# Kernel tuning notes

Hardware: AMD Instinct MI355X
Metric: run time of the kernel (lower is better)

## Reference

```python
import jax, jax.numpy as jnp
import numpy as np

B, S, D, H = 4, 2048, 1024, 16
HD = D // H
FF = 4 * D
EPS = 1e-5


def _layer_norm(x, w, b):
    mu = jnp.mean(x, axis=-1, keepdims=True)
    var = jnp.mean(jnp.square(x - mu), axis=-1, keepdims=True)
    return (x - mu) * jax.lax.rsqrt(var + EPS) * w + b


def setup_inputs() -> dict:
    key = jax.random.key(0)
    ks = jax.random.split(key, 8)
    std = 0.02
    return {
        "x": jax.random.normal(ks[0], (B, S, D), dtype=jnp.float32),
        "ln1_w": jnp.ones((D,), jnp.float32),
        "ln1_b": jnp.zeros((D,), jnp.float32),
        "w_qkv": jax.random.normal(ks[1], (D, 3 * D), dtype=jnp.float32) * std,  # fused QKV, no bias
        "w_proj": jax.random.normal(ks[2], (D, D), dtype=jnp.float32) * std,
        "b_proj": jnp.zeros((D,), jnp.float32),
        "ln2_w": jnp.ones((D,), jnp.float32),
        "ln2_b": jnp.zeros((D,), jnp.float32),
        "w_ff1": jax.random.normal(ks[3], (D, FF), dtype=jnp.float32) * std,
        "b_ff1": jnp.zeros((FF,), jnp.float32),
        "w_ff2": jax.random.normal(ks[4], (FF, D), dtype=jnp.float32) * std,
        "b_ff2": jnp.zeros((D,), jnp.float32),
    }


def reference(x, ln1_w, ln1_b, w_qkv, w_proj, b_proj, ln2_w, ln2_b, w_ff1, b_ff1, w_ff2, b_ff2):
    b, s, d = x.shape
    # --- attention branch (pre-LN) ---
    h = _layer_norm(x, ln1_w, ln1_b)
    kqv = (h @ w_qkv).reshape(b, s, H, HD, 3)  # fused projection, split by last index
    k, q, v = kqv[..., 0], kqv[..., 1], kqv[..., 2]  # each [b, s, H, HD]
    scores = jnp.einsum("bqhd,bkhd->bhqk", q, k) * (HD ** -0.5)  # [b,H,s,s]
    causal = jnp.tril(jnp.ones((s, s), dtype=bool))
    scores = jnp.where(causal, scores, -jnp.inf)
    weights = jax.nn.softmax(scores, axis=-1)
    ctx = jnp.einsum("bhqk,bkhd->bqhd", weights, v).reshape(b, s, d)
    attn_out = ctx @ w_proj + b_proj
    x = x + attn_out
    # --- feed-forward branch (pre-LN) ---
    h = _layer_norm(x, ln2_w, ln2_b)
    ff = jax.nn.gelu(h @ w_ff1 + b_ff1, approximate=False) @ w_ff2 + b_ff2
    return x + ff
```

## Files before the change

kernel.cpp:

```cpp
#include <hip/hip_runtime.h>

typedef unsigned short u16;
typedef unsigned int u32;
typedef __bf16 bf16x8 __attribute__((ext_vector_type(8)));
typedef float f32x4 __attribute__((ext_vector_type(4)));
typedef float f32x16 __attribute__((ext_vector_type(16)));
typedef unsigned short us8 __attribute__((ext_vector_type(8)));
typedef unsigned short us4 __attribute__((ext_vector_type(4)));
typedef unsigned int u32x4 __attribute__((ext_vector_type(4)));

#define B_ 4
#define S_ 2048
#define D_ 1024
#define H_ 16
#define HD_ 64
#define QKS_ 3072
#define EPS_ 1e-5f
#define SCALE_ (0.125f * 1.44269504088896341f)
#define THR_ 3.0f

__device__ __forceinline__ u16 f2bf(float f) {
  unsigned u = __builtin_bit_cast(unsigned, f);
  u = (u + 0x7FFFu + ((u >> 16) & 1u)) >> 16;
  return (u16)u;
}

__device__ __forceinline__ float gelu_f(float x) {
  float u = x * (2.3022388f + 0.10294971f * x * x);
  float te = __builtin_amdgcn_exp2f(u);
  return x - x * __builtin_amdgcn_rcpf(1.0f + te);
}

typedef const __attribute__((address_space(1))) unsigned int* gp1;
typedef __attribute__((address_space(3))) unsigned int* lp3;
__device__ __forceinline__ void gl_lds16(const void* g, void* l) {
  __builtin_amdgcn_global_load_lds((gp1)(unsigned long long)g,
                                   (lp3)(unsigned int)(unsigned long long)l,
                                   16, 0, 0);
}

__device__ __forceinline__ u32 cvtpk_bf16(float lo, float hi) {
  u32 d;
  asm("v_cvt_pk_bf16_f32 %0, %1, %2" : "=v"(d) : "v"(lo), "v"(hi));
  return d;
}
__device__ __forceinline__ void swap32(u32& a, u32& b) {
  asm("v_permlane32_swap_b32 %0, %1" : "+v"(a), "+v"(b));
}

__device__ __forceinline__ f32x16 zero16() {
  f32x16 z;
#pragma unroll
  for (int i = 0; i < 16; i++) z[i] = 0.f;
  return z;
}

__global__ __launch_bounds__(256) void wconv_kernel(const float* __restrict__ W,
                                                    u16* __restrict__ Wt,
                                                    int Kd, int N, int perm) {
  __shared__ u16 tile[32][33];
  int bid = blockIdx.x;
  int nbn = N >> 5;
  int tk = bid / nbn, tn = bid % nbn;
  int tx = threadIdx.x & 31, ty = threadIdx.x >> 5;
#pragma unroll
  for (int i = 0; i < 4; i++) {
    int r = ty + i * 8;
    tile[r][tx] = f2bf(W[(size_t)(tk * 32 + r) * N + tn * 32 + tx]);
  }
  __syncthreads();
#pragma unroll
  for (int i = 0; i < 4; i++) {
    int r = ty + i * 8;
    int orow = tn * 32 + r;
    int prow = perm ? ((orow % 3) << 10) + orow / 3 : orow;
    Wt[(size_t)prow * Kd + tk * 32 + tx] = tile[tx][r];
  }
}

__global__ __launch_bounds__(256) void vtrans_kernel(const u16* __restrict__ kqv,
                                                     u16* __restrict__ Vt) {
  __shared__ u16 tile[64][72];
  int bh = blockIdx.x >> 5;
  int sb = blockIdx.x & 31;
  int b = bh >> 4, h = bh & 15;
  const u16* src = kqv + ((size_t)(b * S_ + sb * 64)) * QKS_ + 2048 + h * 64;
  int r = threadIdx.x >> 2, c0 = (threadIdx.x & 3) * 16;
  *(us8*)&tile[r][c0] = *(const us8*)(src + (size_t)r * QKS_ + c0);
  *(us8*)&tile[r][c0 + 8] = *(const us8*)(src + (size_t)r * QKS_ + c0 + 8);
  __syncthreads();
  u16* dst = Vt + (size_t)bh * HD_ * S_ + sb * 64;
  int hd = threadIdx.x >> 2;
  int s0 = (threadIdx.x & 3) * 16;
  us8 a, bb;
#pragma unroll
  for (int j = 0; j < 8; j++) a[j] = tile[s0 + j][hd];
#pragma unroll
  for (int j = 0; j < 8; j++) bb[j] = tile[s0 + 8 + j][hd];
  *(us8*)(dst + (size_t)hd * S_ + s0) = a;
  *(us8*)(dst + (size_t)hd * S_ + s0 + 8) = bb;
}

__global__ __launch_bounds__(256) void ln_kernel(const float* __restrict__ x,
                                                 const float* __restrict__ w,
                                                 const float* __restrict__ b,
                                                 u16* __restrict__ out) {
  int row = blockIdx.x;
  int t = threadIdx.x;
  int lane = t & 63, wid = t >> 6;
  const float4* xr = (const float4*)(x + (size_t)row * D_);
  float4 v = xr[t];
  float s = v.x + v.y + v.z + v.w;
  float q = v.x * v.x + v.y * v.y + v.z * v.z + v.w * v.w;
#pragma unroll
  for (int off = 1; off < 64; off <<= 1) {
    s += __shfl_xor(s, off);
    q += __shfl_xor(q, off);
  }
  __shared__ float red[8];
  if (lane == 0) { red[wid] = s; red[4 + wid] = q; }
  __syncthreads();
  s = red[0] + red[1] + red[2] + red[3];
  q = red[4] + red[5] + red[6] + red[7];
  float mu = s * (1.0f / D_);
  float var = q * (1.0f / D_) - mu * mu;
  float rs = rsqrtf(var + EPS_);
  int c = t * 4;
  float4 wv = *(const float4*)(w + c);
  float4 bv = *(const float4*)(b + c);
  us4 o;
  o[0] = f2bf((v.x - mu) * rs * wv.x + bv.x);
  o[1] = f2bf((v.y - mu) * rs * wv.y + bv.y);
  o[2] = f2bf((v.z - mu) * rs * wv.z + bv.z);
  o[3] = f2bf((v.w - mu) * rs * wv.w + bv.w);
  *(us4*)(out + (size_t)row * D_ + c) = o;
}

template <int MODE>
__global__ __launch_bounds__(256) void gemm_kernel(
    const u16* __restrict__ A, const u16* __restrict__ Bt,
    const float* __restrict__ bias, const float* __restrict__ res,
    float* __restrict__ Cf, u16* __restrict__ Cb,
    int M, int N, int K) {
  __shared__ __align__(16) u16 Al[128 * 64];
  __shared__ __align__(16) u16 Bl[128 * 64];
  int t = threadIdx.x;
  int nbn = N >> 7;
  int nwg = gridDim.x, cpx = nwg >> 3;
  int bid = (blockIdx.x & 7) * cpx + (blockIdx.x >> 3);
  int nsn = nbn >> 3;
  int st = bid >> 6, u = bid & 63;
  int bm = (st / nsn) * 8 + (u >> 3);
  int bn = (st % nsn) * 8 + (u & 7);
  int lane = t & 63, wid = t >> 6;
  int wm = wid >> 1, wn = wid & 1;
  int lrow = lane & 15, lgr = lane >> 4;
  int sl7 = lrow & 7;
  const u16* Ab = A + (size_t)bm * 128 * K;
  const u16* Bb = Bt + (size_t)bn * 128 * K;
  int sr = lane >> 3;
  int sc = ((lane & 7) ^ sr) << 3;
  const u16* Ag[4];
  const u16* Bg[4];
  u16* Ald[4];
  u16* Bld[4];
#pragma unroll
  for (int j = 0; j < 4; j++) {
    int row0 = (j * 4 + wid) * 8;
    Ag[j] = Ab + (size_t)(row0 + sr) * K + sc;
    Bg[j] = Bb + (size_t)(row0 + sr) * K + sc;
    Ald[j] = &Al[row0 * 64 + lane * 8];
    Bld[j] = &Bl[row0 * 64 + lane * 8];
  }
  f32x4 acc[4][4] = {};
  for (int k0 = 0; k0 < K; k0 += 64) {
#pragma unroll
    for (int j = 0; j < 4; j++) {
      gl_lds16(Ag[j] + k0, Ald[j]);
      gl_lds16(Bg[j] + k0, Bld[j]);
    }
    __syncthreads();
    bf16x8 af[2][4], bfr[2][4];
#pragma unroll
    for (int ks = 0; ks < 2; ks++) {
      int slot = ((ks << 2) | lgr) ^ sl7;
#pragma unroll
      for (int m = 0; m < 4; m++)
        af[ks][m] = *(const bf16x8*)&Al[(wm * 64 + m * 16 + lrow) * 64 + slot * 8];
#pragma unroll
      for (int n = 0; n < 4; n++)
        bfr[ks][n] = *(const bf16x8*)&Bl[(wn * 64 + n * 16 + lrow) * 64 + slot * 8];
    }
    __builtin_amdgcn_s_setprio(1);
#pragma unroll
    for (int m = 0; m < 4; m++)
#pragma unroll
      for (int n = 0; n < 4; n++) {
        acc[m][n] = __builtin_amdgcn_mfma_f32_16x16x32_bf16(af[0][m], bfr[0][n], acc[m][n], 0, 0, 0);
        acc[m][n] = __builtin_amdgcn_mfma_f32_16x16x32_bf16(af[1][m], bfr[1][n], acc[m][n], 0, 0, 0);
      }
    __builtin_amdgcn_s_setprio(0);
    __syncthreads();
  }
#pragma unroll
  for (int n = 0; n < 4; n++) {
    int col = bn * 128 + wn * 64 + n * 16 + lrow;
    float bv = (MODE & 1) ? bias[col] : 0.0f;
#pragma unroll
    for (int m = 0; m < 4; m++)
#pragma unroll
      for (int r = 0; r < 4; r++) {
        int row = bm * 128 + wm * 64 + m * 16 + lgr * 4 + r;
        float v = acc[m][n][r] + bv;
        if (MODE & 2) v = gelu_f(v);
        if (MODE & 4) v += res[(size_t)row * N + col];
        if (MODE & 8) Cb[(size_t)row * N + col] = f2bf(v);
        else          Cf[(size_t)row * N + col] = v;
      }
  }
}

__device__ __forceinline__ void attn_softmax_update(
    f32x16* s, int NSUB_rt, float& mrun, float& lrun, f32x16 (&o)[2], int hi) {
  float pmax = -3.0e38f;
  for (int sub = 0; sub < NSUB_rt; sub++)
#pragma unroll
    for (int r = 0; r < 16; r++) pmax = fmaxf(pmax, s[sub][r]);
  pmax = fmaxf(pmax, __shfl_xor(pmax, 32));
  bool ok = (pmax * SCALE_ <= mrun + THR_);
  if (!__all(ok)) {
    float mnew = fmaxf(mrun, pmax * SCALE_);
    float corr = __builtin_amdgcn_exp2f(mrun - mnew);
    mrun = mnew;
    lrun *= corr;
#pragma unroll
    for (int r = 0; r < 16; r++) {
      float cr = __shfl(corr, ((r & 3) + 8 * (r >> 2)) + 4 * hi);
      o[0][r] *= cr;
      o[1][r] *= cr;
    }
  }
  float m = mrun;
  float lacc = 0.f;
  for (int sub = 0; sub < NSUB_rt; sub++)
#pragma unroll
    for (int r = 0; r < 16; r++) {
      float p = __builtin_amdgcn_exp2f(__builtin_fmaf(s[sub][r], SCALE_, -m));
      s[sub][r] = p;
      lacc += p;
    }
  lrun += lacc;
}

__device__ __forceinline__ void attn_pfrag(const f32x16& s, bf16x8& pa, bf16x8& pb) {
  u32 a0 = cvtpk_bf16(s[0], s[1]);
  u32 a1 = cvtpk_bf16(s[2], s[3]);
  u32 a2 = cvtpk_bf16(s[4], s[5]);
  u32 a3 = cvtpk_bf16(s[6], s[7]);
  swap32(a0, a2);
  swap32(a1, a3);
  u32 b0 = cvtpk_bf16(s[8], s[9]);
  u32 b1 = cvtpk_bf16(s[10], s[11]);
  u32 b2 = cvtpk_bf16(s[12], s[13]);
  u32 b3 = cvtpk_bf16(s[14], s[15]);
  swap32(b0, b2);
  swap32(b1, b3);
  u32x4 fa = {a0, a1, a2, a3};
  u32x4 fb = {b0, b1, b2, b3};
  pa = __builtin_bit_cast(bf16x8, fa);
  pb = __builtin_bit_cast(bf16x8, fb);
}

template <bool MASK>
__device__ __forceinline__ void attn_chunk_tail(
    const u16* __restrict__ Kh, const u16* __restrict__ Vh,
    const bf16x8 (&qf)[4], f32x16 (&o)[2],
    float& mrun, float& lrun, int kb, int qrow, int hi, int ln31) {
  f32x16 s[1];
  f32x16 z = zero16();
  __builtin_amdgcn_s_setprio(1);
#pragma unroll
  for (int ks = 0; ks < 4; ks++) {
    bf16x8 kfr = *(const bf16x8*)(Kh + (size_t)(kb + ln31) * QKS_ + ks * 16 + hi * 8);
    z = __builtin_amdgcn_mfma_f32_32x32x16_bf16(kfr, qf[ks], z, 0, 0, 0);
  }
  __builtin_amdgcn_s_setprio(0);
  if (MASK) {
#pragma unroll
    for (int r = 0; r < 16; r++) {
      int key = kb + (r & 3) + 8 * (r >> 2) + 4 * hi;
      if (key > qrow) z[r] = -3.0e38f;
    }
  }
  s[0] = z;
  attn_softmax_update(s, 1, mrun, lrun, o, hi);
  bf16x8 pa, pb;
  attn_pfrag(s[0], pa, pb);
  __builtin_amdgcn_s_setprio(1);
#pragma unroll
  for (int ht = 0; ht < 2; ht++) {
    const u16* vb = Vh + (size_t)(ht * 32 + ln31) * S_ + kb + hi * 8;
    bf16x8 v1 = *(const bf16x8*)(vb);
    bf16x8 v2 = *(const bf16x8*)(vb + 16);
    o[ht] = __builtin_amdgcn_mfma_f32_32x32x16_bf16(pa, v1, o[ht], 0, 0, 0);
    o[ht] = __builtin_amdgcn_mfma_f32_32x32x16_bf16(pb, v2, o[ht], 0, 0, 0);
  }
  __builtin_amdgcn_s_setprio(0);
}

__global__ __launch_bounds__(256) void attn_kernel(const u16* __restrict__ kqv,
                                                   const u16* __restrict__ Vt,
                                                   u16* __restrict__ ctx) {
  __shared__ __align__(16) u16 Kl[2][64 * 64];
  __shared__ __align__(16) u16 Vl[2][64 * 64];
  int t = threadIdx.x;
  int lane = t & 63, wid = t >> 6;
  int qblk = 15 - (int)(blockIdx.x >> 6);
  int bh = blockIdx.x & 63;
  int b = bh >> 4, h = bh & 15;
  const u16* Qh = kqv + (size_t)b * S_ * QKS_ + 1024 + h * 64;
  const u16* Kh = kqv + (size_t)b * S_ * QKS_ + h * 64;
  const u16* Vh = Vt + (size_t)bh * HD_ * S_;
  int qb = qblk * 128;
  int qbase = qb + wid * 32;
  int ln31 = lane & 31, hi = lane >> 5;
  int qrow = qbase + ln31;
  int l7 = ln31 & 7;

  int srow = t >> 3;
  int sslot = (t & 7) ^ (srow & 7);
  const u16* Ksrc = Kh + (size_t)srow * QKS_ + sslot * 8;
  const u16* Vsrc = Vh + (size_t)srow * S_ + sslot * 8;

  auto stageK = [&](int kb1, int buf) {
    gl_lds16(Ksrc + (size_t)kb1 * QKS_, &Kl[buf][t * 8]);
    gl_lds16(Ksrc + (size_t)(kb1 + 32) * QKS_, &Kl[buf][2048 + t * 8]);
  };
  auto stageV = [&](int kb1, int buf) {
    gl_lds16(Vsrc + kb1, &Vl[buf][t * 8]);
    gl_lds16(Vsrc + (size_t)32 * S_ + kb1, &Vl[buf][2048 + t * 8]);
  };

  bf16x8 qf[4];
#pragma unroll
  for (int ks = 0; ks < 4; ks++)
    qf[ks] = *(const bf16x8*)(Qh + (size_t)qrow * QKS_ + ks * 16 + hi * 8);

  f32x16 o[2] = {zero16(), zero16()};
  float mrun = -1.0e30f, lrun = 0.f;

  int nf64 = qbase >> 6;
  int NT = (qb >> 6) + 2;

  stageK(0, 0);
  stageV(0, 0);
  for (int kt = 0; kt < NT; kt++) {
    int cur = kt & 1;
    if (kt + 1 < NT) {
      int kb1 = (kt + 1) * 64;
      stageK(kb1, cur ^ 1);
      stageV(kb1, cur ^ 1);
      asm volatile("s_waitcnt vmcnt(4)" ::: "memory");
    } else {
      asm volatile("s_waitcnt vmcnt(0)" ::: "memory");
    }
    __builtin_amdgcn_sched_barrier(0);
    __builtin_amdgcn_s_barrier();
    __builtin_amdgcn_sched_barrier(0);
    if (kt < nf64) {
      const u16* Kc = &Kl[cur][0];
      const u16* Vc = &Vl[cur][0];
      f32x16 s[2];
#pragma unroll
      for (int sub = 0; sub < 2; sub++) {
        f32x16 z = zero16();
        __builtin_amdgcn_s_setprio(1);
#pragma unroll
        for (int ks = 0; ks < 4; ks++) {
          int kr = sub * 32 + ln31;
          int sl = (ks * 2 + hi) ^ l7;
          bf16x8 kfr = *(const bf16x8*)&Kc[kr * 64 + sl * 8];
          z = __builtin_amdgcn_mfma_f32_32x32x16_bf16(kfr, qf[ks], z, 0, 0, 0);
        }
        __builtin_amdgcn_s_setprio(0);
        s[sub] = z;
      }
      attn_softmax_update(s, 2, mrun, lrun, o, hi);
#pragma unroll
      for (int sub = 0; sub < 2; sub++) {
        bf16x8 pa, pb;
        attn_pfrag(s[sub], pa, pb);
        __builtin_amdgcn_s_setprio(1);
#pragma unroll
        for (int ht = 0; ht < 2; ht++) {
          int vr = ht * 32 + ln31;
          int s1 = (sub * 4 + hi) ^ (vr & 7);
          int s2 = (sub * 4 + hi + 2) ^ (vr & 7);
          bf16x8 v1 = *(const bf16x8*)&Vc[vr * 64 + s1 * 8];
          bf16x8 v2 = *(const bf16x8*)&Vc[vr * 64 + s2 * 8];
          o[ht] = __builtin_amdgcn_mfma_f32_32x32x16_bf16(pa, v1, o[ht], 0, 0, 0);
          o[ht] = __builtin_amdgcn_mfma_f32_32x32x16_bf16(pb, v2, o[ht], 0, 0, 0);
        }
        __builtin_amdgcn_s_setprio(0);
      }
    }
    __builtin_amdgcn_sched_barrier(0);
    __builtin_amdgcn_s_barrier();
    __builtin_amdgcn_sched_barrier(0);
  }

  if (qbase & 32)
    attn_chunk_tail<false>(Kh, Vh, qf, o, mrun, lrun, qbase - 32, qrow, hi, ln31);
  attn_chunk_tail<true>(Kh, Vh, qf, o, mrun, lrun, qbase, qrow, hi, ln31);

  float l = lrun + __shfl_xor(lrun, 32);
  float inv = 1.0f / l;
#pragma unroll
  for (int r = 0; r < 16; r++) {
    float invr = __shfl(inv, ((r & 3) + 8 * (r >> 2)) + 4 * hi);
    int q = qbase + (r & 3) + 8 * (r >> 2) + 4 * hi;
    size_t base = ((size_t)b * S_ + q) * D_ + h * HD_;
    ctx[base + ln31] = f2bf(o[0][r] * invr);
    ctx[base + 32 + ln31] = f2bf(o[1][r] * invr);
  }
}

extern "C" void kernel_launch(void* const* d_in, const int* in_sizes, int n_in,
                              void* d_out, int out_size, void* d_ws, size_t ws_size,
                              hipStream_t stream) {
  const float* x = (const float*)d_in[0];
  const float* ln1w = (const float*)d_in[1];
  const float* ln1b = (const float*)d_in[2];
  const float* wqkv = (const float*)d_in[3];
  const float* wproj = (const float*)d_in[4];
  const float* bproj = (const float*)d_in[5];
  const float* ln2w = (const float*)d_in[6];
  const float* ln2b = (const float*)d_in[7];
  const float* wff1 = (const float*)d_in[8];
  const float* bff1 = (const float*)d_in[9];
  const float* wff2 = (const float*)d_in[10];
  const float* bff2 = (const float*)d_in[11];

  char* ws = (char*)d_ws;
  u16* wqkvT = (u16*)(ws + 0);
  u16* wprojT = (u16*)(ws + 6291456);
  u16* wff1T = (u16*)(ws + 8388608);
  u16* wff2T = (u16*)(ws + 16777216);
  u16* h1 = (u16*)(ws + 25165824);
  u16* Vt = (u16*)(ws + 25165824);
  u16* kqv = (u16*)(ws + 41943040);
  u16* ctx = (u16*)(ws + 92274688);
  float* x1 = (float*)(ws + 109051904);
  u16* h2 = (u16*)(ws + 142606336);
  u16* g = (u16*)(ws + 25165824);
  float* outp = (float*)d_out;

  wconv_kernel<<<(1024 / 32) * (3072 / 32), 256, 0, stream>>>(wqkv, wqkvT, 1024, 3072, 1);
  wconv_kernel<<<(1024 / 32) * (1024 / 32), 256, 0, stream>>>(wproj, wprojT, 1024, 1024, 0);
  wconv_kernel<<<(1024 / 32) * (4096 / 32), 256, 0, stream>>>(wff1, wff1T, 1024, 4096, 0);
  wconv_kernel<<<(4096 / 32) * (1024 / 32), 256, 0, stream>>>(wff2, wff2T, 4096, 1024, 0);

  ln_kernel<<<8192, 256, 0, stream>>>(x, ln1w, ln1b, h1);
  gemm_kernel<8><<<1536, 256, 0, stream>>>(h1, wqkvT, nullptr, nullptr, nullptr, kqv,
                                           8192, 3072, 1024);
  vtrans_kernel<<<64 * 32, 256, 0, stream>>>(kqv, Vt);
  attn_kernel<<<16 * 64, 256, 0, stream>>>(kqv, Vt, ctx);
  gemm_kernel<5><<<512, 256, 0, stream>>>(ctx, wprojT, bproj, x, x1, nullptr,
                                          8192, 1024, 1024);
  ln_kernel<<<8192, 256, 0, stream>>>(x1, ln2w, ln2b, h2);
  gemm_kernel<11><<<2048, 256, 0, stream>>>(h2, wff1T, bff1, nullptr, nullptr, g,
                                            8192, 4096, 1024);
  gemm_kernel<5><<<512, 256, 0, stream>>>(g, wff2T, bff2, x1, outp, nullptr,
                                          8192, 1024, 4096);
}
```

Measured before the change: 346.2 us.

## Add 8-wave ping-pong GEMM with larger tiles for FFN matmuls

```diff
diff --git a/kernel.cpp b/kernel.cpp
--- a/kernel.cpp
+++ b/kernel.cpp
@@ -220,6 +220,151 @@
   }
 }
 
+#define VWAIT(n) asm volatile("s_waitcnt vmcnt(" #n ")" ::: "memory")
+
+#define LDA(AF, MQ)                                                             \
+  _Pragma("unroll") for (int ks = 0; ks < 2; ks++) {                            \
+    int slot = ((((ks << 2) | lgr) ^ sl7)) * 8;                                 \
+    _Pragma("unroll") for (int m = 0; m < MH; m++)                              \
+      AF[ks][m] = *(const bf16x8*)&Ac[((MQ) * (BM / 2) + wm * (BM / 4) +        \
+                                       m * 16 + lrow) * 64 + slot];             \
+  }
+
+#define LDB(BF, NQ)                                                             \
+  _Pragma("unroll") for (int ks = 0; ks < 2; ks++) {                            \
+    int slot = ((((ks << 2) | lgr) ^ sl7)) * 8;                                 \
+    _Pragma("unroll") for (int nn = 0; nn < 2; nn++)                            \
+      BF[ks][nn] = *(const bf16x8*)&Bc[((NQ) * 128 + wn * 32 + nn * 16 +        \
+                                        lrow) * 64 + slot];                     \
+  }
+
+#define BARR_MFMA(MQ, NQ, AF, BF)                                               \
+  __builtin_amdgcn_s_barrier();                                                 \
+  asm volatile("s_waitcnt lgkmcnt(0)" ::: "memory");                            \
+  __builtin_amdgcn_sched_barrier(0);                                            \
+  __builtin_amdgcn_s_setprio(1);                                                \
+  _Pragma("unroll") for (int m = 0; m < MH; m++)                                \
+    _Pragma("unroll") for (int nn = 0; nn < 2; nn++) {                          \
+      acc[MQ][NQ][m][nn] = __builtin_amdgcn_mfma_f32_16x16x32_bf16(             \
+          AF[0][m], BF[0][nn], acc[MQ][NQ][m][nn], 0, 0, 0);                    \
+      acc[MQ][NQ][m][nn] = __builtin_amdgcn_mfma_f32_16x16x32_bf16(             \
+          AF[1][m], BF[1][nn], acc[MQ][NQ][m][nn], 0, 0, 0);                    \
+    }                                                                           \
+  __builtin_amdgcn_s_setprio(0);                                                \
+  __builtin_amdgcn_s_barrier();
+
+template <int MODE, int BM>
+__global__ __launch_bounds__(512) void gemm8p_kernel(
+    const u16* __restrict__ A, const u16* __restrict__ Bt,
+    const float* __restrict__ bias, const float* __restrict__ res,
+    float* __restrict__ Cf, u16* __restrict__ Cb,
+    int M, int N, int K) {
+  constexpr int LA = BM / 128;
+  constexpr int MH = BM / 64;
+  constexpr int ASZ = BM * 64;
+  constexpr int BSZ = 256 * 64;
+  extern __shared__ __align__(16) u16 sm[];
+  int t = threadIdx.x;
+  int nbn = N >> 8;
+  int nwg = gridDim.x, cpx = nwg >> 3;
+  int bid = (blockIdx.x % 8) * cpx + blockIdx.x / 8;
+  int bm = bid / nbn, bn = bid % nbn;
+  int lane = t & 63, wid = t >> 6;
+  int wm = wid >> 2, wn = wid & 3;
+  int lrow = lane & 15, lgr = lane >> 4;
+  int sl7 = lrow & 7;
+  const u16* Ab = A + (size_t)bm * BM * K;
+  const u16* Bb = Bt + (size_t)bn * 256 * K;
+  int srt = t >> 3;
+  int ssc = (((t & 7) ^ (srt & 7)) << 3);
+  const u16* Asrc = Ab + (size_t)srt * K + ssc;
+  const u16* Bsrc = Bb + (size_t)srt * K + ssc;
+
+  auto stageA = [&](int kt, int bsel, int h) {
+    int k0 = kt * 64;
+    u16* dst = sm + bsel * (ASZ + BSZ) + (h * (BM / 2)) * 64 + t * 8;
+#pragma unroll
+    for (int a = 0; a < LA; a++)
+      gl_lds16(Asrc + (size_t)(h * (BM / 2) + a * 64) * K + k0, dst + a * 4096);
+  };
+  auto stageB = [&](int kt, int bsel, int h) {
+    int k0 = kt * 64;
+    u16* dst = sm + bsel * (ASZ + BSZ) + ASZ + (h * 128) * 64 + t * 8;
+#pragma unroll
+    for (int b2 = 0; b2 < 2; b2++)
+      gl_lds16(Bsrc + (size_t)(h * 128 + b2 * 64) * K + k0, dst + b2 * 4096);
+  };
+
+  f32x4 acc[2][2][MH][2] = {};
+  int NT = K >> 6;
+  stageA(0, 0, 0);
+  stageB(0, 0, 0);
+  stageB(0, 0, 1);
+  stageA(0, 0, 1);
+  if constexpr (BM == 256) VWAIT(4); else VWAIT(3);
+  __builtin_amdgcn_s_barrier();
+  for (int kt = 0; kt < NT - 1; kt++) {
+    int cur = kt & 1, nb = cur ^ 1;
+    const u16* Ac = sm + cur * (ASZ + BSZ);
+    const u16* Bc = Ac + ASZ;
+    bf16x8 af[2][MH], bf[2][2];
+    LDA(af, 0);
+    LDB(bf, 0);
+    stageA(kt + 1, nb, 0);
+    if constexpr (BM == 256) VWAIT(4); else VWAIT(2);
+    BARR_MFMA(0, 0, af, bf);
+    LDB(bf, 1);
+    stageB(kt + 1, nb, 0);
+    if constexpr (BM == 256) VWAIT(4); else VWAIT(3);
+    BARR_MFMA(0, 1, af, bf);
+    LDA(af, 1);
+    stageB(kt + 1, nb, 1);
+    BARR_MFMA(1, 1, af, bf);
+    LDB(bf, 0);
+    stageA(kt + 1, nb, 1);
+    if constexpr (BM == 256) VWAIT(4); else VWAIT(3);
+    BARR_MFMA(1, 0, af, bf);
+  }
+  {
+    int cur = (NT - 1) & 1;
+    const u16* Ac = sm + cur * (ASZ + BSZ);
+    const u16* Bc = Ac + ASZ;
+    bf16x8 af[2][MH], bf[2][2];
+    LDA(af, 0);
+    LDB(bf, 0);
+    if constexpr (BM == 256) VWAIT(2); else VWAIT(1);
+    BARR_MFMA(0, 0, af, bf);
+    LDB(bf, 1);
+    VWAIT(0);
+    BARR_MFMA(0, 1, af, bf);
+    LDA(af, 1);
+    BARR_MFMA(1, 1, af, bf);
+    LDB(bf, 0);
+    BARR_MFMA(1, 0, af, bf);
+  }
+#pragma unroll
+  for (int nq = 0; nq < 2; nq++) {
+#pragma unroll
+    for (int nn = 0; nn < 2; nn++) {
+      int col = bn * 256 + nq * 128 + wn * 32 + nn * 16 + lrow;
+      float bv = (MODE & 1) ? bias[col] : 0.0f;
+#pragma unroll
+      for (int mq = 0; mq < 2; mq++)
+#pragma unroll
+        for (int m = 0; m < MH; m++)
+#pragma unroll
+          for (int r = 0; r < 4; r++) {
+            int row = bm * BM + mq * (BM / 2) + wm * (BM / 4) + m * 16 + lgr * 4 + r;
+            float v = acc[mq][nq][m][nn][r] + bv;
+            if (MODE & 2) v = gelu_f(v);
+            if (MODE & 4) v += res[(size_t)row * N + col];
+            if (MODE & 8) Cb[(size_t)row * N + col] = f2bf(v);
+            else          Cf[(size_t)row * N + col] = v;
+          }
+    }
+  }
+}
+
 __device__ __forceinline__ void attn_softmax_update(
     f32x16* s, int NSUB_rt, float& mrun, float& lrun, f32x16 (&o)[2], int hi) {
   float pmax = -3.0e38f;
@@ -455,6 +600,11 @@
   u16* g = (u16*)(ws + 25165824);
   float* outp = (float*)d_out;
 
+  hipFuncSetAttribute((const void*)gemm8p_kernel<11, 256>,
+                      hipFuncAttributeMaxDynamicSharedMemorySize, 131072);
+  hipFuncSetAttribute((const void*)gemm8p_kernel<5, 128>,
+                      hipFuncAttributeMaxDynamicSharedMemorySize, 98304);
+
   wconv_kernel<<<(1024 / 32) * (3072 / 32), 256, 0, stream>>>(wqkv, wqkvT, 1024, 3072, 1);
   wconv_kernel<<<(1024 / 32) * (1024 / 32), 256, 0, stream>>>(wproj, wprojT, 1024, 1024, 0);
   wconv_kernel<<<(1024 / 32) * (4096 / 32), 256, 0, stream>>>(wff1, wff1T, 1024, 4096, 0);
@@ -468,8 +618,8 @@
   gemm_kernel<5><<<512, 256, 0, stream>>>(ctx, wprojT, bproj, x, x1, nullptr,
                                           8192, 1024, 1024);
   ln_kernel<<<8192, 256, 0, stream>>>(x1, ln2w, ln2b, h2);
-  gemm_kernel<11><<<2048, 256, 0, stream>>>(h2, wff1T, bff1, nullptr, nullptr, g,
-                                            8192, 4096, 1024);
-  gemm_kernel<5><<<512, 256, 0, stream>>>(g, wff2T, bff2, x1, outp, nullptr,
-                                          8192, 1024, 4096);
-}
+  gemm8p_kernel<11, 256><<<512, 512, 131072, stream>>>(h2, wff1T, bff1, nullptr, nullptr, g,
+                                                       8192, 4096, 1024);
+  gemm8p_kernel<5, 128><<<256, 512, 98304, stream>>>(g, wff2T, bff2, x1, outp, nullptr,
+                                                     8192, 1024, 4096);
+}
```

Measured after the change: 351.8 us. No clear change (+1.6%).
